# Performance work log

Measured on AMD Instinct MI355X. Metric: run time of the kernel, lower is better.

Reference implementation:

```python
import jax, jax.numpy as jnp
import numpy as np

HEADS = 8
N_STATE = 512
MAX_SEQ = 2048
DEPTH = N_STATE // HEADS
EPS = 1e-5


def layer_norm(x, g, b):
    mu = jnp.mean(x, axis=-1, keepdims=True)
    var = jnp.mean(jnp.square(x - mu), axis=-1, keepdims=True)
    return (x - mu) * jax.lax.rsqrt(var + EPS) * g + b


def setup_inputs() -> dict:
    key = jax.random.key(0)
    ks = jax.random.split(key, 12)
    B, S = 2, 2048
    x = jax.random.normal(ks[0], (B, S, N_STATE), dtype=jnp.float32)
    # causal additive mask (upper triangle = -1e9)
    mask = jnp.where(jnp.tril(jnp.ones((S, S), dtype=bool)), 0.0, -1e9).astype(jnp.float32)
    sc = 0.02
    Wqkv = jax.random.normal(ks[1], (N_STATE, 3 * N_STATE), dtype=jnp.float32) * sc
    bqkv = jnp.zeros((3 * N_STATE,), dtype=jnp.float32)
    Wproj = jax.random.normal(ks[2], (N_STATE, N_STATE), dtype=jnp.float32) * sc
    bproj = jnp.zeros((N_STATE,), dtype=jnp.float32)
    # xavier-normal-ish relative position embeddings, shape (H, max_seq, depth)
    E = jax.random.normal(ks[3], (HEADS, MAX_SEQ, DEPTH), dtype=jnp.float32) * (2.0 / (MAX_SEQ + DEPTH)) ** 0.5
    g1 = jnp.ones((N_STATE,), dtype=jnp.float32)
    b1 = jnp.zeros((N_STATE,), dtype=jnp.float32)
    g2 = jnp.ones((N_STATE,), dtype=jnp.float32)
    b2 = jnp.zeros((N_STATE,), dtype=jnp.float32)
    W1 = jax.random.normal(ks[4], (N_STATE, 4 * N_STATE), dtype=jnp.float32) * sc
    bm1 = jnp.zeros((4 * N_STATE,), dtype=jnp.float32)
    W2 = jax.random.normal(ks[5], (4 * N_STATE, N_STATE), dtype=jnp.float32) * sc
    bm2 = jnp.zeros((N_STATE,), dtype=jnp.float32)
    return {"x": x, "mask": mask, "Wqkv": Wqkv, "bqkv": bqkv, "Wproj": Wproj,
            "bproj": bproj, "E": E, "g1": g1, "b1": b1, "g2": g2, "b2": b2,
            "W1": W1, "bm1": bm1, "W2": W2, "bm2": bm2}


def relative_attn(q, E):
    # q: [B,H,S,D]; E: [H,max_seq,D] -> rel: [B,H,S,S] via skew trick
    B, H, S, D = q.shape
    Es = E[:, MAX_SEQ - S:]                      # [H,S,D]
    rel = jnp.einsum('bhsd,htd->bhst', q, Es)    # [B,H,S,S]
    rel = jnp.pad(rel, ((0, 0), (0, 0), (0, 0), (1, 0)))  # pad left of last dim
    rel = rel.reshape(B, H, S + 1, S)[:, :, 1:]  # skew: drop first row
    return rel


def reference(x, mask, Wqkv, bqkv, Wproj, bproj, E, g1, b1, g2, b2, W1, bm1, W2, bm2):
    B, S, _ = x.shape
    # --- attention sublayer ---
    a = layer_norm(x, g1, b1)
    qkv = a @ Wqkv + bqkv                        # [B,S,3*n_state]
    q, k, v = jnp.split(qkv, 3, axis=-1)
    def heads(t):
        return t.reshape(B, S, HEADS, DEPTH).transpose(0, 2, 1, 3)  # [B,H,S,D]
    q, k, v = heads(q), heads(k), heads(v)
    w = jnp.einsum('bhsd,bhtd->bhst', q, k) + relative_attn(q, E)
    w = w * (1.0 / jnp.sqrt(jnp.float32(DEPTH)))
    w = w + mask                                  # broadcast [S,S]
    w = jax.nn.softmax(w, axis=-1)
    att = jnp.einsum('bhst,bhtd->bhsd', w, v)
    att = att.transpose(0, 2, 1, 3).reshape(B, S, N_STATE)
    att = att @ Wproj + bproj
    x = x + att
    # --- MLP sublayer ---
    m = layer_norm(x, g2, b2)
    m = jax.nn.gelu(m @ W1 + bm1) @ W2 + bm2
    return x + m
```

## Files before the change

### kernel.cpp

```cpp
#include <hip/hip_runtime.h>
#include <math.h>

typedef unsigned short u16;
typedef unsigned int u32;
using short8 = __attribute__((ext_vector_type(8))) short;
using f32x4  = __attribute__((ext_vector_type(4))) float;

#define SEQ 2048
#define NH 8
#define DM 512
#define DH 64
#define NROWS 4096
#define BATCH 2
#define KVB 128

__device__ __forceinline__ float bf2f(u16 u) {
  union { u32 i; float f; } c; c.i = ((u32)u) << 16; return c.f;
}
__device__ __forceinline__ u16 f2bf(float f) {
  union { float f; u32 i; } c; c.f = f;
  u32 r = c.i + 0x7fffu + ((c.i >> 16) & 1u);
  return (u16)(r >> 16);
}

__device__ __forceinline__ void gll16(const u16* g, u16* l) {
  __builtin_amdgcn_global_load_lds(
      (const __attribute__((address_space(1))) u32*)g,
      (__attribute__((address_space(3))) u32*)l, 16, 0, 0);
}

template<int N> __device__ __forceinline__ void waitcnt_vm() {
  if constexpr (N == 0)      asm volatile("s_waitcnt vmcnt(0)" ::: "memory");
  else if constexpr (N == 4) asm volatile("s_waitcnt vmcnt(4)" ::: "memory");
  else if constexpr (N == 6) asm volatile("s_waitcnt vmcnt(6)" ::: "memory");
  else if constexpr (N == 8) asm volatile("s_waitcnt vmcnt(8)" ::: "memory");
}

__global__ __launch_bounds__(64) void ln_bf16_kernel(
    const float* __restrict__ x, const float* __restrict__ gw,
    const float* __restrict__ bw, u16* __restrict__ out)
{
  int row = blockIdx.x;
  int lane = threadIdx.x;
  const float* xr = x + (size_t)row * DM;
  float4 v0 = ((const float4*)xr)[lane];
  float4 v1 = ((const float4*)xr)[lane + 64];
  float s  = v0.x + v0.y + v0.z + v0.w + v1.x + v1.y + v1.z + v1.w;
  float s2 = v0.x*v0.x + v0.y*v0.y + v0.z*v0.z + v0.w*v0.w
           + v1.x*v1.x + v1.y*v1.y + v1.z*v1.z + v1.w*v1.w;
  #pragma unroll
  for (int m = 1; m < 64; m <<= 1) {
    s  += __shfl_xor(s,  m);
    s2 += __shfl_xor(s2, m);
  }
  float mu   = s * (1.0f / DM);
  float var  = s2 * (1.0f / DM) - mu * mu;
  float rstd = rsqrtf(var + 1e-5f);
  float4 ga = ((const float4*)gw)[lane],      ba = ((const float4*)bw)[lane];
  float4 gb = ((const float4*)gw)[lane + 64], bb = ((const float4*)bw)[lane + 64];
  ushort4 o0, o1;
  o0.x = f2bf((v0.x - mu) * rstd * ga.x + ba.x);
  o0.y = f2bf((v0.y - mu) * rstd * ga.y + ba.y);
  o0.z = f2bf((v0.z - mu) * rstd * ga.z + ba.z);
  o0.w = f2bf((v0.w - mu) * rstd * ga.w + ba.w);
  o1.x = f2bf((v1.x - mu) * rstd * gb.x + bb.x);
  o1.y = f2bf((v1.y - mu) * rstd * gb.y + bb.y);
  o1.z = f2bf((v1.z - mu) * rstd * gb.z + bb.z);
  o1.w = f2bf((v1.w - mu) * rstd * gb.w + bb.w);
  *(ushort4*)&out[(size_t)row * DM + lane * 4]       = o0;
  *(ushort4*)&out[(size_t)row * DM + 256 + lane * 4] = o1;
}

__global__ __launch_bounds__(256) void transpose_cast_kernel(
    const float* __restrict__ W, u16* __restrict__ Wt, int K, int N)
{
  __shared__ float tile[32][33];
  int bn = blockIdx.x * 32, bk = blockIdx.y * 32;
  int tx = threadIdx.x & 31, ty = threadIdx.x >> 5;
  #pragma unroll
  for (int i = 0; i < 32; i += 8)
    tile[ty + i][tx] = W[(size_t)(bk + ty + i) * N + bn + tx];
  __syncthreads();
  #pragma unroll
  for (int i = 0; i < 32; i += 8)
    Wt[(size_t)(bn + ty + i) * K + bk + tx] = f2bf(tile[tx][ty + i]);
}

__global__ __launch_bounds__(256) void cast_bf16_kernel(
    const float* __restrict__ in, u16* __restrict__ out, int n)
{
  int i = (blockIdx.x * 256 + threadIdx.x) * 4;
  if (i >= n) return;
  float4 v = *(const float4*)&in[i];
  ushort4 o;
  o.x = f2bf(v.x); o.y = f2bf(v.y); o.z = f2bf(v.z); o.w = f2bf(v.w);
  *(ushort4*)&out[i] = o;
}

template<int TM, int TN, int MODE>
__global__ __launch_bounds__(256) void gemm_bf16(
    const u16* __restrict__ A, const u16* __restrict__ Bt,
    const float* __restrict__ bias, const float* __restrict__ res,
    float* __restrict__ outF, u16* __restrict__ outB0,
    u16* __restrict__ outB1, u16* __restrict__ outB2,
    int M, int N, int K)
{
  constexpr int MI = TM / 32;
  constexpr int NI = TN / 32;
  constexpr int LOADS = TM / 32 + TN / 32;
  __shared__ u16 sA[2][TM * 64];
  __shared__ u16 sB[2][TN * 64];
  int tid = threadIdx.x;
  int lane = tid & 63, wv = tid >> 6;
  int wm = wv >> 1, wn = wv & 1;
  int g = lane >> 4, l15 = lane & 15;

  int nwg = gridDim.x, lin = blockIdx.x;
  int qq = nwg >> 3;
  int wg = (lin & 7) * qq + (lin >> 3);
  int ntn = N / TN;
  int m0 = (wg / ntn) * TM, n0 = (wg % ntn) * TN;

  auto stage = [&](int buf, int k0) {
    #pragma unroll
    for (int s = 0; s < TM / 32; ++s) {
      int c = s * 256 + tid;
      int row = c >> 3, p = c & 7;
      gll16(&A[(size_t)(m0 + row) * K + k0 + ((p ^ (row & 7)) * 8)],
            &sA[buf][(size_t)(s * 256 + wv * 64) * 8]);
    }
    #pragma unroll
    for (int s = 0; s < TN / 32; ++s) {
      int c = s * 256 + tid;
      int row = c >> 3, p = c & 7;
      gll16(&Bt[(size_t)(n0 + row) * K + k0 + ((p ^ (row & 7)) * 8)],
            &sB[buf][(size_t)(s * 256 + wv * 64) * 8]);
    }
  };

  f32x4 acc[MI][NI] = {};
  stage(0, 0);

  int nk = K / 64;
  for (int kt = 0; kt < nk; ++kt) {
    int cur = kt & 1;
    __syncthreads();
    if (kt + 1 < nk) {
      stage(cur ^ 1, (kt + 1) * 64);
      waitcnt_vm<LOADS>();
    } else {
      waitcnt_vm<0>();
    }
    __syncthreads();
    #pragma unroll
    for (int kk = 0; kk < 2; ++kk) {
      short8 af[MI], bfr[NI];
      #pragma unroll
      for (int i = 0; i < MI; ++i) {
        int row = wm * (TM / 2) + i * 16 + l15;
        af[i] = *(const short8*)&sA[cur][row * 64 + (((4 * kk + g) ^ (row & 7)) * 8)];
      }
      #pragma unroll
      for (int i = 0; i < NI; ++i) {
        int row = wn * (TN / 2) + i * 16 + l15;
        bfr[i] = *(const short8*)&sB[cur][row * 64 + (((4 * kk + g) ^ (row & 7)) * 8)];
      }
      #pragma unroll
      for (int mi = 0; mi < MI; ++mi)
        #pragma unroll
        for (int ni = 0; ni < NI; ++ni)
          acc[mi][ni] = __builtin_amdgcn_mfma_f32_16x16x32_bf16(af[mi], bfr[ni], acc[mi][ni], 0, 0, 0);
    }
  }

  #pragma unroll
  for (int mi = 0; mi < MI; ++mi) {
    #pragma unroll
    for (int ni = 0; ni < NI; ++ni) {
      #pragma unroll
      for (int r = 0; r < 4; ++r) {
        int grow = m0 + wm * (TM / 2) + mi * 16 + g * 4 + r;
        int gcol = n0 + wn * (TN / 2) + ni * 16 + l15;
        float val = acc[mi][ni][r] + bias[gcol];
        if (MODE == 0) {
          int part = gcol >> 9, c = gcol & 511;
          int hh = c >> 6, dd = c & 63;
          int bb = grow >> 11, ss = grow & 2047;
          if (part == 0) {
            size_t dst = (((size_t)(bb * NH + hh)) * SEQ + ss) * DH + dd;
            outB0[dst] = f2bf(val * 0.18033688011112042f);
          } else if (part == 1) {
            size_t dst = (((size_t)(bb * NH + hh)) * SEQ + ss) * DH + dd;
            outB1[dst] = f2bf(val);
          } else {
            size_t dst = (((size_t)(bb * NH + hh)) * DH + dd) * SEQ + ss;
            outB2[dst] = f2bf(val);
          }
        } else if (MODE == 1 || MODE == 3) {
          size_t idx = (size_t)grow * DM + gcol;
          outF[idx] = val + res[idx];
        } else {
          float t = val;
          float inner = 0.7978845608028654f * (t + 0.044715f * t * t * t);
          float gl = 0.5f * t * (1.0f + tanhf(inner));
          outB0[(size_t)grow * N + gcol] = f2bf(gl);
        }
      }
    }
  }
}

__global__ __launch_bounds__(256, 2) void attn_kernel(
    const u16* __restrict__ Q, const u16* __restrict__ Kb,
    const u16* __restrict__ Vb, const u16* __restrict__ Eb,
    u16* __restrict__ Ob)
{
  __shared__ u16 sK[KVB * 64];
  __shared__ u16 sVt[2][64 * KVB];
  __shared__ u16 sP[4][16 * 64];
  __shared__ float sM[2][32];
  __shared__ float sS[2][32];

  int tid = threadIdx.x, lane = tid & 63, wv = tid >> 6;
  int wr = wv & 1, wc = wv >> 1;
  int g = lane >> 4, l15 = lane & 15;
  int lin = blockIdx.x;
  int bh   = (lin & 7) * 2 + ((lin >> 3) & 1);
  int tile = 63 - (lin >> 4);
  int hh = bh & (NH - 1), bb = bh >> 3;
  int NIT = tile / 4 + 1;

  const u16* Qh = Q  + (size_t)bh * SEQ * DH;
  const u16* Kh = Kb + (size_t)bh * SEQ * DH;
  const u16* Vt = Vb + (size_t)bh * DH * SEQ;
  const u16* Eh = Eb + (size_t)hh * SEQ * DH;

  int vrow = tid >> 4;
  int vsrc = ((tid & 15) ^ vrow) * 8;
  auto stageV = [&](int buf, int tb) {
    #pragma unroll
    for (int s = 0; s < 4; ++s) {
      gll16(&Vt[(size_t)(s * 16 + vrow) * SEQ + tb + vsrc],
            &sVt[buf][(size_t)(s * 256 + wv * 64) * 8]);
    }
  };

  #pragma unroll
  for (int s = 0; s < 4; ++s) {
    int c = s * 256 + tid, t = c >> 3, pc = c & 7;
    gll16(&Kh[(size_t)t * DH + ((pc ^ (t & 7)) * 8)],
          &sK[(size_t)(s * 256 + wv * 64) * 8]);
  }
  stageV(0, 0);
  asm volatile("s_waitcnt vmcnt(0)" ::: "memory");
  __syncthreads();

  int sw = tile * 32 + wr * 16;
  short8 qf[2];
  qf[0] = *(const short8*)&Qh[(size_t)(sw + l15) * DH + g * 8];
  qf[1] = *(const short8*)&Qh[(size_t)(sw + l15) * DH + g * 8 + 32];

  f32x4 o[4] = {};
  float mrow[4] = {-1e30f, -1e30f, -1e30f, -1e30f};
  float lsum[4] = {};

  float* sO = (float*)&sP[0][0];

  for (int it = 0; it < NIT; ++it) {
    int t0 = it * KVB, cur = it & 1;
    bool pre = (it + 1 < NIT);
    int tb = (it + 1) * KVB;

    f32x4 accS[4];
    #pragma unroll
    for (int ni = 0; ni < 4; ++ni) {
      int row = wc * 64 + ni * 16 + l15;
      short8 k0 = *(const short8*)&sK[row * 64 + ((g ^ (row & 7)) * 8)];
      short8 k1 = *(const short8*)&sK[row * 64 + (((4 + g) ^ (row & 7)) * 8)];
      f32x4 z = {};
      z = __builtin_amdgcn_mfma_f32_16x16x32_bf16(qf[0], k0, z, 0, 0, 0);
      z = __builtin_amdgcn_mfma_f32_16x16x32_bf16(qf[1], k1, z, 0, 0, 0);
      accS[ni] = z;
    }

    int jbase = 2032 - sw + t0 + wc * 64;
    f32x4 accR[5];
    #pragma unroll
    for (int nb = 0; nb < 5; ++nb) {
      int j = jbase + nb * 16 + l15; if (j > 2047) j = 2047;
      short8 e0 = *(const short8*)&Eh[(size_t)j * DH + g * 8];
      short8 e1 = *(const short8*)&Eh[(size_t)j * DH + 32 + g * 8];
      f32x4 z = {};
      z = __builtin_amdgcn_mfma_f32_16x16x32_bf16(qf[0], e0, z, 0, 0, 0);
      z = __builtin_amdgcn_mfma_f32_16x16x32_bf16(qf[1], e1, z, 0, 0, 0);
      accR[nb] = z;
    }

    bool needMask = (t0 + wc * 64 + 63 > sw);
    #pragma unroll
    for (int r = 0; r < 4; ++r) {
      int srow = g * 4 + r;
      int dsh = 15 - srow + l15;
      int srcl = (lane & 48) + (dsh & 15);
      float sh[5];
      #pragma unroll
      for (int nb = 0; nb < 5; ++nb) sh[nb] = __shfl(accR[nb][r], srcl);
      bool cy = dsh >= 16;
      #pragma unroll
      for (int ni = 0; ni < 4; ++ni) {
        float rel = cy ? sh[ni + 1] : sh[ni];
        float val = accS[ni][r] + rel;
        if (needMask && (t0 + wc * 64 + ni * 16 + l15 > sw + srow)) val = -1e30f;
        accS[ni][r] = val;
      }
    }

    float lmax[4];
    #pragma unroll
    for (int r = 0; r < 4; ++r) {
      float tm = fmaxf(fmaxf(accS[0][r], accS[1][r]), fmaxf(accS[2][r], accS[3][r]));
      tm = fmaxf(tm, __shfl_xor(tm, 1));
      tm = fmaxf(tm, __shfl_xor(tm, 2));
      tm = fmaxf(tm, __shfl_xor(tm, 4));
      tm = fmaxf(tm, __shfl_xor(tm, 8));
      lmax[r] = tm;
    }
    if (l15 == 0) {
      #pragma unroll
      for (int r = 0; r < 4; ++r) sM[wc][wr * 16 + g * 4 + r] = lmax[r];
    }
    __syncthreads();
    if (pre) {
      #pragma unroll
      for (int s = 0; s < 4; ++s) {
        int c = s * 256 + tid, t = c >> 3, pc = c & 7;
        gll16(&Kh[(size_t)(tb + t) * DH + ((pc ^ (t & 7)) * 8)],
              &sK[(size_t)(s * 256 + wv * 64) * 8]);
      }
      stageV(cur ^ 1, tb);
    }
    float4 om = *(float4*)&sM[wc ^ 1][wr * 16 + g * 4];

    float sesav[4], lscl[4];
    #pragma unroll
    for (int r = 0; r < 4; ++r) {
      float gm = fmaxf(lmax[r], ((float*)&om)[r]);
      float mnew = fmaxf(mrow[r], gm);
      lscl[r] = exp2f(mrow[r] - mnew);
      mrow[r] = mnew;
      float se = 0.f;
      #pragma unroll
      for (int ni = 0; ni < 4; ++ni) {
        float pe = exp2f(accS[ni][r] - mnew);
        accS[ni][r] = pe;
        se += pe;
      }
      se += __shfl_xor(se, 1); se += __shfl_xor(se, 2);
      se += __shfl_xor(se, 4); se += __shfl_xor(se, 8);
      sesav[r] = se;
      o[0][r] *= lscl[r]; o[1][r] *= lscl[r]; o[2][r] *= lscl[r]; o[3][r] *= lscl[r];
    }
    if (l15 == 0) {
      #pragma unroll
      for (int r = 0; r < 4; ++r) sS[wc][wr * 16 + g * 4 + r] = sesav[r];
    }

    #pragma unroll
    for (int ni = 0; ni < 4; ++ni)
      #pragma unroll
      for (int r = 0; r < 4; ++r) {
        int srow = g * 4 + r;
        int chunk = (ni * 2 + (l15 >> 3)) ^ (srow & 7);
        sP[wv][srow * 64 + chunk * 8 + (l15 & 7)] = f2bf(accS[ni][r]);
      }
    asm volatile("s_waitcnt lgkmcnt(0)" ::: "memory");
    __builtin_amdgcn_sched_barrier(0);
    #pragma unroll
    for (int kk = 0; kk < 2; ++kk) {
      short8 pf = *(const short8*)&sP[wv][l15 * 64 + (((kk * 4 + g) ^ (l15 & 7)) * 8)];
      #pragma unroll
      for (int nb = 0; nb < 4; ++nb) {
        int row = nb * 16 + l15;
        int ck = wc * 8 + kk * 4 + g;
        short8 vf = *(const short8*)&sVt[cur][row * KVB + ((ck ^ l15) * 8)];
        o[nb] = __builtin_amdgcn_mfma_f32_16x16x32_bf16(pf, vf, o[nb], 0, 0, 0);
      }
    }

    __syncthreads();
    float4 os = *(float4*)&sS[wc ^ 1][wr * 16 + g * 4];
    #pragma unroll
    for (int r = 0; r < 4; ++r)
      lsum[r] = lsum[r] * lscl[r] + sesav[r] + ((float*)&os)[r];
  }

  {
    if (wc == 1) {
      #pragma unroll
      for (int r = 0; r < 4; ++r) {
        float rl = 1.0f / lsum[r];
        #pragma unroll
        for (int nb = 0; nb < 4; ++nb)
          sO[wr * 1024 + (g * 4 + r) * 64 + nb * 16 + l15] = o[nb][r] * rl;
      }
    }
    __syncthreads();
    if (wc == 0) {
      #pragma unroll
      for (int r = 0; r < 4; ++r) {
        float rl = 1.0f / lsum[r];
        int ss = sw + g * 4 + r;
        #pragma unroll
        for (int nb = 0; nb < 4; ++nb) {
          float val = o[nb][r] * rl + sO[wr * 1024 + (g * 4 + r) * 64 + nb * 16 + l15];
          Ob[((size_t)(bb * SEQ + ss)) * DM + hh * DH + nb * 16 + l15] = f2bf(val);
        }
      }
    }
  }
}

extern "C" void kernel_launch(void* const* d_in, const int* in_sizes, int n_in,
                              void* d_out, int out_size, void* d_ws, size_t ws_size,
                              hipStream_t stream) {
  const float* x     = (const float*)d_in[0];
  const float* Wqkv  = (const float*)d_in[2];
  const float* bqkv  = (const float*)d_in[3];
  const float* Wproj = (const float*)d_in[4];
  const float* bproj = (const float*)d_in[5];
  const float* E     = (const float*)d_in[6];
  const float* g1    = (const float*)d_in[7];
  const float* b1    = (const float*)d_in[8];
  const float* g2    = (const float*)d_in[9];
  const float* b2    = (const float*)d_in[10];
  const float* W1    = (const float*)d_in[11];
  const float* bm1   = (const float*)d_in[12];
  const float* W2    = (const float*)d_in[13];
  const float* bm2   = (const float*)d_in[14];
  float* out = (float*)d_out;

  char* ws = (char*)d_ws;
  size_t off = 0;
  auto alloc = [&](size_t bytes) {
    void* p = ws + off;
    off += (bytes + 255) & ~(size_t)255;
    return p;
  };
  u16* a_bf   = (u16*)alloc((size_t)NROWS * DM * 2);
  u16* q_bf   = (u16*)alloc((size_t)NROWS * DM * 2);
  u16* k_bf   = (u16*)alloc((size_t)NROWS * DM * 2);
  u16* v_bf   = (u16*)alloc((size_t)NROWS * DM * 2);
  u16* att_bf = (u16*)alloc((size_t)NROWS * DM * 2);
  float* y    = (float*)alloc((size_t)NROWS * DM * 4);
  u16* h_bf   = (u16*)alloc((size_t)NROWS * 2048 * 2);
  u16* WqkvT  = (u16*)alloc((size_t)1536 * 512 * 2);
  u16* WprojT = (u16*)alloc((size_t)512 * 512 * 2);
  u16* W1T    = (u16*)alloc((size_t)2048 * 512 * 2);
  u16* W2T    = (u16*)alloc((size_t)512 * 2048 * 2);
  u16* E_bf   = (u16*)alloc((size_t)NH * SEQ * DH * 2);

  transpose_cast_kernel<<<dim3(1536 / 32, 512 / 32), 256, 0, stream>>>(Wqkv, WqkvT, 512, 1536);
  transpose_cast_kernel<<<dim3(512 / 32, 512 / 32), 256, 0, stream>>>(Wproj, WprojT, 512, 512);
  transpose_cast_kernel<<<dim3(2048 / 32, 512 / 32), 256, 0, stream>>>(W1, W1T, 512, 2048);
  transpose_cast_kernel<<<dim3(512 / 32, 2048 / 32), 256, 0, stream>>>(W2, W2T, 2048, 512);
  cast_bf16_kernel<<<(NH * SEQ * DH) / (256 * 4), 256, 0, stream>>>(E, E_bf, NH * SEQ * DH);

  ln_bf16_kernel<<<NROWS, 64, 0, stream>>>(x, g1, b1, a_bf);
  gemm_bf16<64, 128, 0><<<(NROWS / 64) * (1536 / 128), 256, 0, stream>>>(
      a_bf, WqkvT, bqkv, nullptr, nullptr, q_bf, k_bf, v_bf, NROWS, 1536, 512);
  attn_kernel<<<1024, 256, 0, stream>>>(q_bf, k_bf, v_bf, E_bf, att_bf);
  gemm_bf16<64, 64, 1><<<(NROWS / 64) * (512 / 64), 256, 0, stream>>>(
      att_bf, WprojT, bproj, x, y, nullptr, nullptr, nullptr, NROWS, 512, 512);
  ln_bf16_kernel<<<NROWS, 64, 0, stream>>>(y, g2, b2, a_bf);
  gemm_bf16<64, 128, 2><<<(NROWS / 64) * (2048 / 128), 256, 0, stream>>>(
      a_bf, W1T, bm1, nullptr, nullptr, h_bf, nullptr, nullptr, NROWS, 2048, 512);
  gemm_bf16<64, 64, 3><<<(NROWS / 64) * (512 / 64), 256, 0, stream>>>(
      h_bf, W2T, bm2, y, out, nullptr, nullptr, nullptr, NROWS, 512, 2048);
}
```

Before: 168.7 us.

## Decouple attention softmax across column waves and merge weight-prep kernels

The attention kernel now keeps a separate running max and row sum per column-half wave and merges the two halves only once at the end. This removes the per-iteration shared-memory exchange of max and sum. Row sums are computed with an MFMA against a vector of ones, and the cross-lane max uses DPP row rotates instead of shuffles, with the initial max clamped to -64. The next K/V prefetch is issued earlier, right after QK^T, and the four transpose kernels plus the E cast are fused into one prep launch. The -64 initial max and the bf16-rounded probabilities in the sum could shift numerics slightly.

After: 149.2 us. 1.13x faster.

```diff
diff --git a/kernel.cpp b/kernel.cpp
--- a/kernel.cpp
+++ b/kernel.cpp
@@ -34,6 +34,12 @@
   else if constexpr (N == 4) asm volatile("s_waitcnt vmcnt(4)" ::: "memory");
   else if constexpr (N == 6) asm volatile("s_waitcnt vmcnt(6)" ::: "memory");
   else if constexpr (N == 8) asm volatile("s_waitcnt vmcnt(8)" ::: "memory");
+}
+
+template<int N> __device__ __forceinline__ float fmax_ror(float x) {
+  int y = __builtin_amdgcn_update_dpp(0, __builtin_bit_cast(int, x),
+                                      0x120 + N, 0xF, 0xF, true);
+  return fmaxf(x, __builtin_bit_cast(float, y));
 }
 
 __global__ __launch_bounds__(64) void ln_bf16_kernel(
@@ -71,11 +77,29 @@
   *(ushort4*)&out[(size_t)row * DM + 256 + lane * 4] = o1;
 }
 
-__global__ __launch_bounds__(256) void transpose_cast_kernel(
-    const float* __restrict__ W, u16* __restrict__ Wt, int K, int N)
+__global__ __launch_bounds__(256) void prep_kernel(
+    const float* __restrict__ Wqkv, const float* __restrict__ Wproj,
+    const float* __restrict__ W1, const float* __restrict__ W2,
+    const float* __restrict__ E,
+    u16* __restrict__ WqkvT, u16* __restrict__ WprojT,
+    u16* __restrict__ W1T, u16* __restrict__ W2T, u16* __restrict__ E_bf)
 {
+  int b = blockIdx.x;
+  if (b >= 3072) {
+    int i = ((b - 3072) * 256 + threadIdx.x) * 4;
+    float4 v = *(const float4*)&E[i];
+    ushort4 o;
+    o.x = f2bf(v.x); o.y = f2bf(v.y); o.z = f2bf(v.z); o.w = f2bf(v.w);
+    *(ushort4*)&E_bf[i] = o;
+    return;
+  }
+  const float* W; u16* Wt; int K, N, b2, nx;
+  if (b < 768)       { W = Wqkv;  Wt = WqkvT;  K = 512;  N = 1536; b2 = b;        nx = 48; }
+  else if (b < 1024) { W = Wproj; Wt = WprojT; K = 512;  N = 512;  b2 = b - 768;  nx = 16; }
+  else if (b < 2048) { W = W1;    Wt = W1T;    K = 512;  N = 2048; b2 = b - 1024; nx = 64; }
+  else               { W = W2;    Wt = W2T;    K = 2048; N = 512;  b2 = b - 2048; nx = 16; }
   __shared__ float tile[32][33];
-  int bn = blockIdx.x * 32, bk = blockIdx.y * 32;
+  int bn = (b2 % nx) * 32, bk = (b2 / nx) * 32;
   int tx = threadIdx.x & 31, ty = threadIdx.x >> 5;
   #pragma unroll
   for (int i = 0; i < 32; i += 8)
@@ -84,17 +108,6 @@
   #pragma unroll
   for (int i = 0; i < 32; i += 8)
     Wt[(size_t)(bn + ty + i) * K + bk + tx] = f2bf(tile[tx][ty + i]);
-}
-
-__global__ __launch_bounds__(256) void cast_bf16_kernel(
-    const float* __restrict__ in, u16* __restrict__ out, int n)
-{
-  int i = (blockIdx.x * 256 + threadIdx.x) * 4;
-  if (i >= n) return;
-  float4 v = *(const float4*)&in[i];
-  ushort4 o;
-  o.x = f2bf(v.x); o.y = f2bf(v.y); o.z = f2bf(v.z); o.w = f2bf(v.w);
-  *(ushort4*)&out[i] = o;
 }
 
 template<int TM, int TN, int MODE>
@@ -261,8 +274,10 @@
   qf[1] = *(const short8*)&Qh[(size_t)(sw + l15) * DH + g * 8 + 32];
 
   f32x4 o[4] = {};
-  float mrow[4] = {-1e30f, -1e30f, -1e30f, -1e30f};
-  float lsum[4] = {};
+  f32x4 osum = {};
+  float mrow[4] = {-64.f, -64.f, -64.f, -64.f};
+  const short8 ones = {0x3F80, 0x3F80, 0x3F80, 0x3F80,
+                       0x3F80, 0x3F80, 0x3F80, 0x3F80};
 
   float* sO = (float*)&sP[0][0];
 
@@ -283,6 +298,17 @@
       accS[ni] = z;
     }
 
+    __syncthreads();
+    if (pre) {
+      #pragma unroll
+      for (int s = 0; s < 4; ++s) {
+        int c = s * 256 + tid, t = c >> 3, pc = c & 7;
+        gll16(&Kh[(size_t)(tb + t) * DH + ((pc ^ (t & 7)) * 8)],
+              &sK[(size_t)(s * 256 + wv * 64) * 8]);
+      }
+      stageV(cur ^ 1, tb);
+    }
+
     int jbase = 2032 - sw + t0 + wc * 64;
     f32x4 accR[5];
     #pragma unroll
@@ -315,54 +341,21 @@
       }
     }
 
-    float lmax[4];
     #pragma unroll
     for (int r = 0; r < 4; ++r) {
       float tm = fmaxf(fmaxf(accS[0][r], accS[1][r]), fmaxf(accS[2][r], accS[3][r]));
-      tm = fmaxf(tm, __shfl_xor(tm, 1));
-      tm = fmaxf(tm, __shfl_xor(tm, 2));
-      tm = fmaxf(tm, __shfl_xor(tm, 4));
-      tm = fmaxf(tm, __shfl_xor(tm, 8));
-      lmax[r] = tm;
-    }
-    if (l15 == 0) {
-      #pragma unroll
-      for (int r = 0; r < 4; ++r) sM[wc][wr * 16 + g * 4 + r] = lmax[r];
-    }
-    __syncthreads();
-    if (pre) {
-      #pragma unroll
-      for (int s = 0; s < 4; ++s) {
-        int c = s * 256 + tid, t = c >> 3, pc = c & 7;
-        gll16(&Kh[(size_t)(tb + t) * DH + ((pc ^ (t & 7)) * 8)],
-              &sK[(size_t)(s * 256 + wv * 64) * 8]);
-      }
-      stageV(cur ^ 1, tb);
-    }
-    float4 om = *(float4*)&sM[wc ^ 1][wr * 16 + g * 4];
-
-    float sesav[4], lscl[4];
-    #pragma unroll
-    for (int r = 0; r < 4; ++r) {
-      float gm = fmaxf(lmax[r], ((float*)&om)[r]);
-      float mnew = fmaxf(mrow[r], gm);
-      lscl[r] = exp2f(mrow[r] - mnew);
+      tm = fmax_ror<8>(tm);
+      tm = fmax_ror<4>(tm);
+      tm = fmax_ror<2>(tm);
+      tm = fmax_ror<1>(tm);
+      float mnew = fmaxf(mrow[r], tm);
+      float scl = exp2f(mrow[r] - mnew);
       mrow[r] = mnew;
-      float se = 0.f;
-      #pragma unroll
-      for (int ni = 0; ni < 4; ++ni) {
-        float pe = exp2f(accS[ni][r] - mnew);
-        accS[ni][r] = pe;
-        se += pe;
-      }
-      se += __shfl_xor(se, 1); se += __shfl_xor(se, 2);
-      se += __shfl_xor(se, 4); se += __shfl_xor(se, 8);
-      sesav[r] = se;
-      o[0][r] *= lscl[r]; o[1][r] *= lscl[r]; o[2][r] *= lscl[r]; o[3][r] *= lscl[r];
-    }
-    if (l15 == 0) {
-      #pragma unroll
-      for (int r = 0; r < 4; ++r) sS[wc][wr * 16 + g * 4 + r] = sesav[r];
+      #pragma unroll
+      for (int ni = 0; ni < 4; ++ni)
+        accS[ni][r] = exp2f(accS[ni][r] - mnew);
+      o[0][r] *= scl; o[1][r] *= scl; o[2][r] *= scl; o[3][r] *= scl;
+      osum[r] *= scl;
     }
 
     #pragma unroll
@@ -378,6 +371,7 @@
     #pragma unroll
     for (int kk = 0; kk < 2; ++kk) {
       short8 pf = *(const short8*)&sP[wv][l15 * 64 + (((kk * 4 + g) ^ (l15 & 7)) * 8)];
+      osum = __builtin_amdgcn_mfma_f32_16x16x32_bf16(pf, ones, osum, 0, 0, 0);
       #pragma unroll
       for (int nb = 0; nb < 4; ++nb) {
         int row = nb * 16 + l15;
@@ -388,31 +382,44 @@
     }
 
     __syncthreads();
-    float4 os = *(float4*)&sS[wc ^ 1][wr * 16 + g * 4];
-    #pragma unroll
-    for (int r = 0; r < 4; ++r)
-      lsum[r] = lsum[r] * lscl[r] + sesav[r] + ((float*)&os)[r];
   }
 
   {
+    if (l15 == 0) {
+      #pragma unroll
+      for (int r = 0; r < 4; ++r) {
+        sM[wc][wr * 16 + g * 4 + r] = mrow[r];
+        sS[wc][wr * 16 + g * 4 + r] = osum[r];
+      }
+    }
+    __syncthreads();
+    float4 om = *(float4*)&sM[wc ^ 1][wr * 16 + g * 4];
+    float4 ol = *(float4*)&sS[wc ^ 1][wr * 16 + g * 4];
+    float fac[4];
+    #pragma unroll
+    for (int r = 0; r < 4; ++r) {
+      float mg = fmaxf(mrow[r], ((float*)&om)[r]);
+      float w  = exp2f(mrow[r] - mg);
+      float wo = exp2f(((float*)&om)[r] - mg);
+      float den = osum[r] * w + ((float*)&ol)[r] * wo;
+      fac[r] = w / den;
+    }
+    __syncthreads();
     if (wc == 1) {
       #pragma unroll
-      for (int r = 0; r < 4; ++r) {
-        float rl = 1.0f / lsum[r];
+      for (int r = 0; r < 4; ++r)
         #pragma unroll
         for (int nb = 0; nb < 4; ++nb)
-          sO[wr * 1024 + (g * 4 + r) * 64 + nb * 16 + l15] = o[nb][r] * rl;
-      }
+          sO[wr * 1024 + (g * 4 + r) * 64 + nb * 16 + l15] = o[nb][r] * fac[r];
     }
     __syncthreads();
     if (wc == 0) {
       #pragma unroll
       for (int r = 0; r < 4; ++r) {
-        float rl = 1.0f / lsum[r];
         int ss = sw + g * 4 + r;
         #pragma unroll
         for (int nb = 0; nb < 4; ++nb) {
-          float val = o[nb][r] * rl + sO[wr * 1024 + (g * 4 + r) * 64 + nb * 16 + l15];
+          float val = o[nb][r] * fac[r] + sO[wr * 1024 + (g * 4 + r) * 64 + nb * 16 + l15];
           Ob[((size_t)(bb * SEQ + ss)) * DM + hh * DH + nb * 16 + l15] = f2bf(val);
         }
       }
@@ -459,11 +466,8 @@
   u16* W2T    = (u16*)alloc((size_t)512 * 2048 * 2);
   u16* E_bf   = (u16*)alloc((size_t)NH * SEQ * DH * 2);
 
-  transpose_cast_kernel<<<dim3(1536 / 32, 512 / 32), 256, 0, stream>>>(Wqkv, WqkvT, 512, 1536);
-  transpose_cast_kernel<<<dim3(512 / 32, 512 / 32), 256, 0, stream>>>(Wproj, WprojT, 512, 512);
-  transpose_cast_kernel<<<dim3(2048 / 32, 512 / 32), 256, 0, stream>>>(W1, W1T, 512, 2048);
-  transpose_cast_kernel<<<dim3(512 / 32, 2048 / 32), 256, 0, stream>>>(W2, W2T, 2048, 512);
-  cast_bf16_kernel<<<(NH * SEQ * DH) / (256 * 4), 256, 0, stream>>>(E, E_bf, NH * SEQ * DH);
+  prep_kernel<<<4096, 256, 0, stream>>>(Wqkv, Wproj, W1, W2, E,
+                                        WqkvT, WprojT, W1T, W2T, E_bf);
 
   ln_bf16_kernel<<<NROWS, 64, 0, stream>>>(x, g1, b1, a_bf);
   gemm_bf16<64, 128, 0><<<(NROWS / 64) * (1536 / 128), 256, 0, stream>>>(
```
